# Kernel optimization log

Measured on AMD Instinct MI355X. Metric: run time of the kernel, lower is better.

The kernel has to match this reference:

```python
import jax, jax.numpy as jnp
import numpy as np

NUM_QUERIES = 300


def setup_inputs() -> dict:
    key = jax.random.key(0)
    ks = jax.random.split(key, 16)
    B, C, NC = 16, 256, 80
    s = 0.02
    return {
        "s3": jax.random.normal(ks[0], (B, C, 128, 128), jnp.float32),
        "s4": jax.random.normal(ks[1], (B, C, 64, 64), jnp.float32),
        "s5": jax.random.normal(ks[2], (B, C, 32, 32), jnp.float32),
        "w_score": jax.random.normal(ks[3], (C, NC), jnp.float32) * s,
        "b_score": jnp.zeros((NC,), jnp.float32),
        "w1": jax.random.normal(ks[4], (C, C), jnp.float32) * s,
        "b1": jnp.zeros((C,), jnp.float32),
        "w2": jax.random.normal(ks[5], (C, C), jnp.float32) * s,
        "b2": jnp.zeros((C,), jnp.float32),
        "w3": jax.random.normal(ks[6], (C, 4), jnp.float32) * s,
        "b3": jnp.zeros((4,), jnp.float32),
        "w_proj": jax.random.normal(ks[7], (C, C), jnp.float32) * s,
        "b_proj": jnp.zeros((C,), jnp.float32),
    }


def _flatten(feats):
    # each feat [B,C,H,W] -> [B,H*W,C]; concat over levels
    mems = [f.reshape(f.shape[0], f.shape[1], -1).transpose(0, 2, 1) for f in feats]
    return jnp.concatenate(mems, axis=1)


def reference(s3, s4, s5, w_score, b_score, w1, b1, w2, b2, w3, b3, w_proj, b_proj):
    memory = _flatten([s3, s4, s5])  # [B, N, C]

    # encoder heads
    enc_logits = memory @ w_score + b_score                      # [B, N, num_classes]
    h = jax.nn.relu(memory @ w1 + b1)
    h = jax.nn.relu(h @ w2 + b2)
    enc_boxes = h @ w3 + b3                                      # [B, N, 4]

    # top-k query selection: sigmoid -> per-token max class score -> topk -> gather
    scores = jax.nn.sigmoid(enc_logits).max(axis=-1)             # [B, N]
    topk_scores, topk_idx = jax.lax.top_k(scores, NUM_QUERIES)   # [B, K]
    topk_mem = jnp.take_along_axis(memory, topk_idx[:, :, None], axis=1)    # [B, K, C]
    topk_boxes = jnp.take_along_axis(enc_boxes, topk_idx[:, :, None], axis=1)  # [B, K, 4]

    tgt = topk_mem @ w_proj + b_proj                             # [B, K, C]
    ref_points = jax.nn.sigmoid(topk_boxes)                      # [B, K, 4]

    return (tgt, ref_points, enc_logits, jax.nn.sigmoid(enc_boxes), topk_idx, topk_scores)
```

## Files before the change

### kernel.cpp

```cpp
#include <hip/hip_runtime.h>
#include <math.h>

#define BATCH 16
#define CDIM 256
#define NCLS 80
#define N3 16384
#define N4 4096
#define N5 1024
#define NTOK 21504
#define KQ 300
#define KSEL 512
#define CANDMAX 1024

typedef __attribute__((ext_vector_type(8))) short short8;
typedef __attribute__((ext_vector_type(4))) float floatx4;
typedef __attribute__((ext_vector_type(16))) float floatx16;
typedef unsigned short ushort_t;

__device__ __forceinline__ float sigmoidf_(float x) {
    return 1.0f / (1.0f + __expf(-x));
}

__device__ __forceinline__ ushort_t f2bf(float f) {
    unsigned int x = __float_as_uint(f);
    unsigned int r = (x + 0x7FFFu + ((x >> 16) & 1u)) >> 16;
    return (ushort_t)r;
}

__device__ __forceinline__ float bf2f(ushort_t u) {
    return __uint_as_float((unsigned int)u << 16);
}

__device__ __forceinline__ void locate_level(
    int n, int bb,
    const float* __restrict__ s3, const float* __restrict__ s4, const float* __restrict__ s5,
    const float*& src, int& nloc, int& lsz)
{
    if (n < N3)           { src = s3 + (size_t)bb * CDIM * N3; nloc = n;           lsz = N3; }
    else if (n < N3 + N4) { src = s4 + (size_t)bb * CDIM * N4; nloc = n - N3;      lsz = N4; }
    else                  { src = s5 + (size_t)bb * CDIM * N5; nloc = n - N3 - N4; lsz = N5; }
}

__global__ __launch_bounds__(256) void prep_weights(
    const float* __restrict__ w1, const float* __restrict__ w2,
    const float* __restrict__ w_score,
    ushort_t* __restrict__ wPk)
{
    const int c = blockIdx.x;
    for (int i = threadIdx.x; i < 8192; i += 256) {
        const int f = i >> 9;
        const int e = i & 511;
        const int ln = e >> 3;
        const int j = e & 7;
        const int col = ln & 31;
        const int k = 16 * f + (ln >> 5) * 8 + j;
        float v;
        if (c < 3) {
            const int cc = 32 * c + col;
            v = (cc < NCLS) ? w_score[k * NCLS + cc] : 0.f;
        } else if (c < 11) {
            v = w1[k * 256 + (32 * (c - 3) + col)];
        } else {
            v = w2[k * 256 + (32 * (c - 11) + col)];
        }
        wPk[(size_t)c * 8192 + i] = f2bf(v);
    }
}

__global__ __launch_bounds__(256) void enc_mfma_kernel(
    const float* __restrict__ s3, const float* __restrict__ s4, const float* __restrict__ s5,
    const ushort_t* __restrict__ wPk,
    const float* __restrict__ b_score, const float* __restrict__ b1,
    const float* __restrict__ b2,
    const float* __restrict__ w3, const float* __restrict__ b3,
    float* __restrict__ out_logits, float* __restrict__ out_sboxes,
    float* __restrict__ ws_scores)
{
    __shared__ __align__(16) ushort_t ldsA[256 * 68];
    __shared__ __align__(16) float w3_s[256 * 4];
    __shared__ float smax_s[2][64];

    const int t = threadIdx.x;
    const int lane = t & 63;
    const int w = t >> 6;
    const int tw = w & 1;
    const int cw = w >> 1;
    const int ln = lane & 31;
    const int half = lane >> 5;

    const int bb = blockIdx.x / 336;
    const int tile = blockIdx.x % 336;
    const int T0 = tile * 64;

    const float* src; int nloc, lsz;
    locate_level(T0, bb, s3, s4, s5, src, nloc, lsz);

    {
        const int tokq = t & 15;
        const int kr = t >> 4;
        #pragma unroll
        for (int p = 0; p < 16; ++p) {
            const int k = p * 16 + kr;
            const float4 v = *(const float4*)(src + (size_t)k * lsz + nloc + 4 * tokq);
            const unsigned int lo = (unsigned int)f2bf(v.x) | ((unsigned int)f2bf(v.y) << 16);
            const unsigned int hi = (unsigned int)f2bf(v.z) | ((unsigned int)f2bf(v.w) << 16);
            *(uint2*)&ldsA[k * 68 + 4 * tokq] = make_uint2(lo, hi);
        }
        *(float4*)&w3_s[t * 4] = *(const float4*)(w3 + t * 4);
    }
    __syncthreads();

    short8 af[16];
    #pragma unroll
    for (int f = 0; f < 16; ++f) {
        short8 a;
        #pragma unroll
        for (int j = 0; j < 8; ++j)
            a[j] = (short)ldsA[(16 * f + 8 * half + j) * 68 + 32 * tw + ln];
        af[f] = a;
    }
    __syncthreads();

    const int gtok0 = bb * NTOK + T0 + 32 * tw;

    float smaxr[16];
    #pragma unroll
    for (int r = 0; r < 16; ++r) smaxr[r] = -1e30f;

    for (int c = cw; c < 11; c += 2) {
        const ushort_t* bp = wPk + (size_t)c * 8192;
        floatx16 acc = {0.f,0.f,0.f,0.f,0.f,0.f,0.f,0.f,0.f,0.f,0.f,0.f,0.f,0.f,0.f,0.f};
        #pragma unroll
        for (int fh = 0; fh < 2; ++fh) {
            short8 bf[8];
            #pragma unroll
            for (int f2 = 0; f2 < 8; ++f2)
                bf[f2] = *(const short8*)&bp[(8 * fh + f2) * 512 + lane * 8];
            #pragma unroll
            for (int f2 = 0; f2 < 8; ++f2)
                acc = __builtin_amdgcn_mfma_f32_32x32x16_bf16(af[8 * fh + f2], bf[f2], acc, 0, 0, 0);
        }
        if (c < 3) {
            const int col = 32 * c + ln;
            const bool valid = col < NCLS;
            const float bias = valid ? b_score[col] : 0.f;
            #pragma unroll
            for (int r = 0; r < 16; ++r) {
                const int row = (r & 3) + 8 * (r >> 2) + 4 * half;
                const float v = acc[r] + bias;
                if (valid) {
                    out_logits[(size_t)(gtok0 + row) * NCLS + col] = v;
                    smaxr[r] = fmaxf(smaxr[r], v);
                }
            }
        } else {
            const int col = 32 * (c - 3) + ln;
            const float bias = b1[col];
            #pragma unroll
            for (int r = 0; r < 16; ++r) {
                const int row = (r & 3) + 8 * (r >> 2) + 4 * half;
                const int tok = 32 * tw + row;
                const float v = fmaxf(acc[r] + bias, 0.f);
                ldsA[tok * 256 + ((((col >> 3) ^ (row & 7)) << 3) | (col & 7))] = f2bf(v);
            }
        }
    }

    #pragma unroll
    for (int r = 0; r < 16; ++r) {
        float m = smaxr[r];
        m = fmaxf(m, __shfl_xor(m, 1));
        m = fmaxf(m, __shfl_xor(m, 2));
        m = fmaxf(m, __shfl_xor(m, 4));
        m = fmaxf(m, __shfl_xor(m, 8));
        m = fmaxf(m, __shfl_xor(m, 16));
        if (ln == 0) {
            const int row = (r & 3) + 8 * (r >> 2) + 4 * half;
            smax_s[cw][32 * tw + row] = m;
        }
    }
    __syncthreads();

    if (t < 64) {
        const float m = fmaxf(smax_s[0][t], smax_s[1][t]);
        ws_scores[bb * NTOK + T0 + t] = sigmoidf_(m);
    }

    {
        const int tok = 32 * tw + ln;
        #pragma unroll
        for (int f = 0; f < 16; ++f) {
            const int chnk = 2 * f + half;
            af[f] = *(const short8*)&ldsA[tok * 256 + ((chnk ^ (tok & 7)) << 3)];
        }
    }
    __syncthreads();

    for (int c = 11 + cw; c < 19; c += 2) {
        const ushort_t* bp = wPk + (size_t)c * 8192;
        floatx16 acc = {0.f,0.f,0.f,0.f,0.f,0.f,0.f,0.f,0.f,0.f,0.f,0.f,0.f,0.f,0.f,0.f};
        #pragma unroll
        for (int fh = 0; fh < 2; ++fh) {
            short8 bf[8];
            #pragma unroll
            for (int f2 = 0; f2 < 8; ++f2)
                bf[f2] = *(const short8*)&bp[(8 * fh + f2) * 512 + lane * 8];
            #pragma unroll
            for (int f2 = 0; f2 < 8; ++f2)
                acc = __builtin_amdgcn_mfma_f32_32x32x16_bf16(af[8 * fh + f2], bf[f2], acc, 0, 0, 0);
        }
        const int col = 32 * (c - 11) + ln;
        const float bias = b2[col];
        #pragma unroll
        for (int r = 0; r < 16; ++r) {
            const int row = (r & 3) + 8 * (r >> 2) + 4 * half;
            const int tok = 32 * tw + row;
            const float v = fmaxf(acc[r] + bias, 0.f);
            ldsA[tok * 256 + ((((col >> 3) ^ (row & 7)) << 3) | (col & 7))] = f2bf(v);
        }
    }
    __syncthreads();

    {
        const int tok = t >> 2;
        const int j = t & 3;
        float acc = b3[j];
        #pragma unroll
        for (int ch = 0; ch < 32; ++ch) {
            const short8 v = *(const short8*)&ldsA[tok * 256 + ((ch ^ (tok & 7)) << 3)];
            #pragma unroll
            for (int jj = 0; jj < 8; ++jj)
                acc = fmaf(bf2f((ushort_t)v[jj]), w3_s[(ch * 8 + jj) * 4 + j], acc);
        }
        out_sboxes[(size_t)(bb * NTOK + T0 + tok) * 4 + j] = sigmoidf_(acc);
    }
}

__global__ __launch_bounds__(256) void select_kernel(
    const float* __restrict__ scores,
    int* __restrict__ cand_idx, unsigned int* __restrict__ cand_cnt)
{
    const int bb = blockIdx.x;
    const int t = threadIdx.x;
    const int lane = t & 63;
    const float* s = scores + bb * NTOK;

    __shared__ unsigned int hist[256];
    __shared__ unsigned int prefix_s, rem_s, cnt_s;

    unsigned int prefix = 0, mask = 0;
    int remaining = KSEL;
    for (int pass = 0; pass < 4; pass++) {
        const int shift = 24 - 8 * pass;
        hist[t] = 0;
        __syncthreads();
        for (int n = t; n < NTOK; n += 256) {
            const unsigned int key = __float_as_uint(s[n]);
            const bool pred = ((key & mask) == prefix);
            const unsigned int bin = pred ? ((key >> shift) & 255u) : 0xFFFFu;
            const unsigned long long alive = __ballot(pred);
            if (alive) {
                const int leader = __builtin_ctzll(alive);
                const unsigned int lbin = (unsigned int)__shfl((int)bin, leader);
                const unsigned long long match = __ballot(pred && bin == lbin);
                if (lane == leader)
                    atomicAdd(&hist[lbin], (unsigned int)__popcll(match));
                else if (pred && bin != lbin)
                    atomicAdd(&hist[bin], 1u);
            }
        }
        __syncthreads();
        if (t == 0) {
            int rem = remaining; unsigned int bsel = 0;
            for (int bin = 255; bin >= 0; bin--) {
                int c = (int)hist[bin];
                if (c >= rem) { bsel = (unsigned int)bin; break; }
                rem -= c;
            }
            prefix_s = prefix | (bsel << shift);
            rem_s = (unsigned int)rem;
        }
        __syncthreads();
        prefix = prefix_s; remaining = (int)rem_s;
        mask |= 0xFFu << shift;
        __syncthreads();
    }
    const unsigned int Tkey = prefix;

    if (t == 0) cnt_s = 0;
    __syncthreads();
    for (int n = t; n < NTOK; n += 256) {
        const unsigned int key = __float_as_uint(s[n]);
        const bool pred = (key >= Tkey);
        const unsigned long long m = __ballot(pred);
        if (m) {
            const int leader = __builtin_ctzll(m);
            unsigned int base = 0;
            if (lane == leader) base = atomicAdd(&cnt_s, (unsigned int)__popcll(m));
            base = (unsigned int)__shfl((int)base, leader);
            if (pred) {
                const unsigned int pos =
                    base + (unsigned int)__popcll(m & ((1ull << lane) - 1ull));
                if (pos < CANDMAX) cand_idx[bb * CANDMAX + pos] = n;
            }
        }
    }
    __syncthreads();
    if (t == 0) {
        unsigned int c = cnt_s; if (c > CANDMAX) c = CANDMAX;
        cand_cnt[bb] = c;
    }
}

__global__ __launch_bounds__(256) void rescore_kernel(
    const float* __restrict__ s3, const float* __restrict__ s4, const float* __restrict__ s5,
    const float* __restrict__ w_score, const float* __restrict__ b_score,
    const int* __restrict__ cand_idx, const unsigned int* __restrict__ cand_cnt,
    double* __restrict__ cand_score)
{
    __shared__ float mrow[4][CDIM];
    const int t = threadIdx.x;
    const int w = t >> 6;
    const int lane = t & 63;
    const int bb = blockIdx.x / (CANDMAX / 4);
    const int c  = (blockIdx.x % (CANDMAX / 4)) * 4 + w;
    const unsigned int cnt = cand_cnt[bb];
    const bool active = (unsigned int)c < cnt;

    int n = 0;
    if (active) n = cand_idx[bb * CANDMAX + c];
    if (active) {
        const float* src; int nloc, lsz;
        locate_level(n, bb, s3, s4, s5, src, nloc, lsz);
        #pragma unroll
        for (int j = 0; j < 4; j++)
            mrow[w][4 * lane + j] = src[(size_t)(4 * lane + j) * lsz + nloc];
    }
    __syncthreads();

    if (active) {
        double acc0 = (double)b_score[lane];
        double acc1 = (lane < 16) ? (double)b_score[64 + lane] : -1.0e300;
        for (int k = 0; k < CDIM; k++) {
            const double m = (double)mrow[w][k];
            acc0 += m * (double)w_score[k * NCLS + lane];
            if (lane < 16) acc1 += m * (double)w_score[k * NCLS + 64 + lane];
        }
        double mx = fmax(acc0, acc1);
        mx = fmax(mx, __shfl_xor(mx, 1));
        mx = fmax(mx, __shfl_xor(mx, 2));
        mx = fmax(mx, __shfl_xor(mx, 4));
        mx = fmax(mx, __shfl_xor(mx, 8));
        mx = fmax(mx, __shfl_xor(mx, 16));
        mx = fmax(mx, __shfl_xor(mx, 32));
        if (lane == 0) cand_score[bb * CANDMAX + c] = mx;
    }
}

__global__ __launch_bounds__(256) void fsort_kernel(
    const double* __restrict__ cand_score, const int* __restrict__ cand_idx,
    const unsigned int* __restrict__ cand_cnt,
    float* __restrict__ out_idx_f, float* __restrict__ out_scores,
    int* __restrict__ ws_idx)
{
    __shared__ double ss[CANDMAX];
    __shared__ int    ii[CANDMAX];
    const int bb = blockIdx.x;
    const int t = threadIdx.x;
    const unsigned int cnt = cand_cnt[bb];

    for (int i = t; i < CANDMAX; i += 256) {
        if ((unsigned int)i < cnt) {
            ss[i] = cand_score[bb * CANDMAX + i];
            ii[i] = cand_idx[bb * CANDMAX + i];
        } else {
            ss[i] = -1.0e300;
            ii[i] = 0x7FFFFFFF;
        }
    }
    __syncthreads();

    for (int ksz = 2; ksz <= CANDMAX; ksz <<= 1) {
        for (int j = ksz >> 1; j > 0; j >>= 1) {
            #pragma unroll
            for (int p = 0; p < CANDMAX / 256; p++) {
                const int i = p * 256 + t;
                const int ixj = i ^ j;
                if (ixj > i) {
                    double sa = ss[i], sb = ss[ixj];
                    int ia = ii[i], ib = ii[ixj];
                    const bool up = ((i & ksz) != 0);
                    const bool agtb = (sa > sb) || (sa == sb && ia < ib);
                    if (agtb == up) { ss[i] = sb; ss[ixj] = sa; ii[i] = ib; ii[ixj] = ia; }
                }
            }
            __syncthreads();
        }
    }

    for (int q = t; q < KQ; q += 256) {
        const double x = ss[q];
        const int idx = ii[q];
        out_scores[bb * KQ + q] = (float)(1.0 / (1.0 + exp(-x)));
        out_idx_f[bb * KQ + q] = (float)idx;
        ws_idx[bb * KQ + q] = idx;
    }
}

__global__ __launch_bounds__(256) void gather_proj_kernel(
    const float* __restrict__ s3, const float* __restrict__ s4, const float* __restrict__ s5,
    const float* __restrict__ w_proj, const float* __restrict__ b_proj,
    const int* __restrict__ ws_idx, const float* __restrict__ out_sboxes,
    float* __restrict__ out_tgt, float* __restrict__ out_ref)
{
    __shared__ float memQ[20][CDIM];
    __shared__ int qidx[20];
    const int t = threadIdx.x;
    const int bb = blockIdx.x / 15;
    const int tile = blockIdx.x % 15;
    const int q0 = tile * 20;

    if (t < 20) qidx[t] = ws_idx[bb * KQ + q0 + t];
    __syncthreads();

    #pragma unroll 4
    for (int q = 0; q < 20; q++) {
        const int n = qidx[q];
        const float* src; int nloc, lsz;
        locate_level(n, bb, s3, s4, s5, src, nloc, lsz);
        memQ[q][t] = src[(size_t)t * lsz + nloc];
    }
    __syncthreads();

    const int j = t;
    float acc[20];
    #pragma unroll
    for (int q = 0; q < 20; q++) acc[q] = b_proj[j];
    for (int k = 0; k < CDIM; k++) {
        const float w = w_proj[(size_t)k * CDIM + j];
        #pragma unroll
        for (int q = 0; q < 20; q++) acc[q] = fmaf(memQ[q][k], w, acc[q]);
    }
    #pragma unroll
    for (int q = 0; q < 20; q++)
        out_tgt[(size_t)(bb * KQ + q0 + q) * CDIM + j] = acc[q];

    if (t < 80) {
        const int q = t >> 2, c = t & 3;
        const int n = qidx[q];
        out_ref[(size_t)(bb * KQ + q0 + q) * 4 + c] =
            out_sboxes[(size_t)(bb * NTOK + n) * 4 + c];
    }
}

extern "C" void kernel_launch(void* const* d_in, const int* in_sizes, int n_in,
                              void* d_out, int out_size, void* d_ws, size_t ws_size,
                              hipStream_t stream) {
    const float* s3      = (const float*)d_in[0];
    const float* s4      = (const float*)d_in[1];
    const float* s5      = (const float*)d_in[2];
    const float* w_score = (const float*)d_in[3];
    const float* b_score = (const float*)d_in[4];
    const float* w1      = (const float*)d_in[5];
    const float* b1      = (const float*)d_in[6];
    const float* w2      = (const float*)d_in[7];
    const float* b2      = (const float*)d_in[8];
    const float* w3      = (const float*)d_in[9];
    const float* b3      = (const float*)d_in[10];
    const float* w_proj  = (const float*)d_in[11];
    const float* b_proj  = (const float*)d_in[12];

    float* out = (float*)d_out;
    float* out_tgt    = out;
    float* out_ref    = out + 1228800;
    float* out_logits = out + 1248000;
    float* out_sboxes = out + 28773120;
    float* out_idx    = out + 30149376;
    float* out_scores = out + 30154176;

    char* ws = (char*)d_ws;
    float*        ws_scores  = (float*)(ws + 0);
    double*       cand_score = (double*)(ws + 1376256);
    int*          cand_idx   = (int*)(ws + 1507328);
    unsigned int* cand_cnt   = (unsigned int*)(ws + 1572864);
    int*          ws_idx     = (int*)(ws + 1573120);
    ushort_t*     wPk        = (ushort_t*)(ws + 1592576);

    prep_weights<<<19, 256, 0, stream>>>(w1, w2, w_score, wPk);

    enc_mfma_kernel<<<BATCH * 336, 256, 0, stream>>>(
        s3, s4, s5, wPk, b_score, b1, b2, w3, b3,
        out_logits, out_sboxes, ws_scores);

    select_kernel<<<BATCH, 256, 0, stream>>>(ws_scores, cand_idx, cand_cnt);

    rescore_kernel<<<BATCH * (CANDMAX / 4), 256, 0, stream>>>(
        s3, s4, s5, w_score, b_score, cand_idx, cand_cnt, cand_score);

    fsort_kernel<<<BATCH, 256, 0, stream>>>(
        cand_score, cand_idx, cand_cnt, out_idx, out_scores, ws_idx);

    gather_proj_kernel<<<BATCH * 15, 256, 0, stream>>>(
        s3, s4, s5, w_proj, b_proj, ws_idx, out_sboxes, out_tgt, out_ref);
}
```

Measured before the change: 1.038 ms.

## Double encoder token tile, reuse weight fragments across two MFMA tiles, MFMA box head

The encoder kernel now handles 128 tokens per block instead of 64. Each wave loads its activation fragments straight from global memory into registers, skipping the LDS transpose, and applies every loaded weight fragment to two 32-token MFMA tiles, which halves weight traffic per token. The final 256→4 box projection now runs as a single zero-padded MFMA, using a packed bf16 w3 copy built in prep_weights, in place of the scalar FMA loop. The costs are much higher register pressure (launch bounds set to 2 blocks per CU), half as many blocks, and strided scalar global loads for the activations.

New measurement: 1.315 ms. 26.8% more time.

```diff
diff --git a/kernel.cpp b/kernel.cpp
--- a/kernel.cpp
+++ b/kernel.cpp
@@ -11,11 +11,15 @@
 #define KQ 300
 #define KSEL 512
 #define CANDMAX 1024
+#define TBLK 128
+#define NBLK 168
 
 typedef __attribute__((ext_vector_type(8))) short short8;
-typedef __attribute__((ext_vector_type(4))) float floatx4;
 typedef __attribute__((ext_vector_type(16))) float floatx16;
 typedef unsigned short ushort_t;
+
+#define ZEROV {0.f,0.f,0.f,0.f,0.f,0.f,0.f,0.f,0.f,0.f,0.f,0.f,0.f,0.f,0.f,0.f}
+#define H1S(tok, col) (((tok) << 8) + (((((col) >> 3) ^ ((tok) & 7)) << 3) | ((col) & 7)))
 
 __device__ __forceinline__ float sigmoidf_(float x) {
     return 1.0f / (1.0f + __expf(-x));
@@ -27,10 +31,6 @@
     return (ushort_t)r;
 }
 
-__device__ __forceinline__ float bf2f(ushort_t u) {
-    return __uint_as_float((unsigned int)u << 16);
-}
-
 __device__ __forceinline__ void locate_level(
     int n, int bb,
     const float* __restrict__ s3, const float* __restrict__ s4, const float* __restrict__ s5,
@@ -43,42 +43,43 @@
 
 __global__ __launch_bounds__(256) void prep_weights(
     const float* __restrict__ w1, const float* __restrict__ w2,
-    const float* __restrict__ w_score,
-    ushort_t* __restrict__ wPk)
+    const float* __restrict__ w_score, const float* __restrict__ w3,
+    ushort_t* __restrict__ wPk, ushort_t* __restrict__ w3Pk)
 {
     const int c = blockIdx.x;
     for (int i = threadIdx.x; i < 8192; i += 256) {
         const int f = i >> 9;
         const int e = i & 511;
-        const int ln = e >> 3;
+        const int lni = e >> 3;
         const int j = e & 7;
-        const int col = ln & 31;
-        const int k = 16 * f + (ln >> 5) * 8 + j;
+        const int col = lni & 31;
+        const int k = 16 * f + (lni >> 5) * 8 + j;
         float v;
         if (c < 3) {
             const int cc = 32 * c + col;
             v = (cc < NCLS) ? w_score[k * NCLS + cc] : 0.f;
         } else if (c < 11) {
             v = w1[k * 256 + (32 * (c - 3) + col)];
+        } else if (c < 19) {
+            v = w2[k * 256 + (32 * (c - 11) + col)];
         } else {
-            v = w2[k * 256 + (32 * (c - 11) + col)];
-        }
-        wPk[(size_t)c * 8192 + i] = f2bf(v);
-    }
-}
-
-__global__ __launch_bounds__(256) void enc_mfma_kernel(
+            v = (col < 4) ? w3[k * 4 + col] : 0.f;
+        }
+        ushort_t* dst = (c < 19) ? (wPk + (size_t)c * 8192) : w3Pk;
+        dst[i] = f2bf(v);
+    }
+}
+
+__global__ __launch_bounds__(256, 2) void enc_mfma_kernel(
     const float* __restrict__ s3, const float* __restrict__ s4, const float* __restrict__ s5,
-    const ushort_t* __restrict__ wPk,
+    const ushort_t* __restrict__ wPk, const ushort_t* __restrict__ w3Pk,
     const float* __restrict__ b_score, const float* __restrict__ b1,
-    const float* __restrict__ b2,
-    const float* __restrict__ w3, const float* __restrict__ b3,
+    const float* __restrict__ b2, const float* __restrict__ b3,
     float* __restrict__ out_logits, float* __restrict__ out_sboxes,
     float* __restrict__ ws_scores)
 {
-    __shared__ __align__(16) ushort_t ldsA[256 * 68];
-    __shared__ __align__(16) float w3_s[256 * 4];
-    __shared__ float smax_s[2][64];
+    __shared__ __align__(16) ushort_t h1b[TBLK * 256];
+    __shared__ float smax_s[2][TBLK];
 
     const int t = threadIdx.x;
     const int lane = t & 63;
@@ -88,151 +89,167 @@
     const int ln = lane & 31;
     const int half = lane >> 5;
 
-    const int bb = blockIdx.x / 336;
-    const int tile = blockIdx.x % 336;
-    const int T0 = tile * 64;
+    const int bb = blockIdx.x / NBLK;
+    const int tile = blockIdx.x % NBLK;
+    const int T0 = tile * TBLK;
 
     const float* src; int nloc, lsz;
     locate_level(T0, bb, s3, s4, s5, src, nloc, lsz);
 
-    {
-        const int tokq = t & 15;
-        const int kr = t >> 4;
-        #pragma unroll
-        for (int p = 0; p < 16; ++p) {
-            const int k = p * 16 + kr;
-            const float4 v = *(const float4*)(src + (size_t)k * lsz + nloc + 4 * tokq);
-            const unsigned int lo = (unsigned int)f2bf(v.x) | ((unsigned int)f2bf(v.y) << 16);
-            const unsigned int hi = (unsigned int)f2bf(v.z) | ((unsigned int)f2bf(v.w) << 16);
-            *(uint2*)&ldsA[k * 68 + 4 * tokq] = make_uint2(lo, hi);
-        }
-        *(float4*)&w3_s[t * 4] = *(const float4*)(w3 + t * 4);
-    }
-    __syncthreads();
-
-    short8 af[16];
-    #pragma unroll
-    for (int f = 0; f < 16; ++f) {
-        short8 a;
-        #pragma unroll
-        for (int j = 0; j < 8; ++j)
-            a[j] = (short)ldsA[(16 * f + 8 * half + j) * 68 + 32 * tw + ln];
-        af[f] = a;
-    }
-    __syncthreads();
-
-    const int gtok0 = bb * NTOK + T0 + 32 * tw;
-
-    float smaxr[16];
-    #pragma unroll
-    for (int r = 0; r < 16; ++r) smaxr[r] = -1e30f;
-
-    for (int c = cw; c < 11; c += 2) {
-        const ushort_t* bp = wPk + (size_t)c * 8192;
-        floatx16 acc = {0.f,0.f,0.f,0.f,0.f,0.f,0.f,0.f,0.f,0.f,0.f,0.f,0.f,0.f,0.f,0.f};
-        #pragma unroll
-        for (int fh = 0; fh < 2; ++fh) {
-            short8 bf[8];
-            #pragma unroll
-            for (int f2 = 0; f2 < 8; ++f2)
-                bf[f2] = *(const short8*)&bp[(8 * fh + f2) * 512 + lane * 8];
-            #pragma unroll
-            for (int f2 = 0; f2 < 8; ++f2)
-                acc = __builtin_amdgcn_mfma_f32_32x32x16_bf16(af[8 * fh + f2], bf[f2], acc, 0, 0, 0);
-        }
-        if (c < 3) {
-            const int col = 32 * c + ln;
-            const bool valid = col < NCLS;
-            const float bias = valid ? b_score[col] : 0.f;
+    short8 af[2][16];
+    #pragma unroll
+    for (int tt = 0; tt < 2; ++tt) {
+        const float* colp = src + (size_t)(nloc + 64 * tw + 32 * tt + ln);
+        #pragma unroll
+        for (int f = 0; f < 16; ++f) {
+            const size_t kb = (size_t)(16 * f + 8 * half);
+            float r[8];
+            #pragma unroll
+            for (int j = 0; j < 8; ++j) r[j] = colp[(kb + j) * (size_t)lsz];
+            short8 a;
+            #pragma unroll
+            for (int j = 0; j < 8; ++j) a[j] = (short)f2bf(r[j]);
+            af[tt][f] = a;
+        }
+    }
+
+    const int gt00 = bb * NTOK + T0;
+
+    auto mm2 = [&](const ushort_t* bp, floatx16& a0, floatx16& a1) {
+        short8 blo[8], bhi[8];
+        #pragma unroll
+        for (int f2 = 0; f2 < 8; ++f2)
+            blo[f2] = *(const short8*)&bp[(size_t)f2 * 512 + lane * 8];
+        #pragma unroll
+        for (int f2 = 0; f2 < 8; ++f2)
+            bhi[f2] = *(const short8*)&bp[(size_t)(8 + f2) * 512 + lane * 8];
+        #pragma unroll
+        for (int f2 = 0; f2 < 8; ++f2) {
+            a0 = __builtin_amdgcn_mfma_f32_32x32x16_bf16(af[0][f2], blo[f2], a0, 0, 0, 0);
+            a1 = __builtin_amdgcn_mfma_f32_32x32x16_bf16(af[1][f2], blo[f2], a1, 0, 0, 0);
+        }
+        #pragma unroll
+        for (int f2 = 0; f2 < 8; ++f2) {
+            a0 = __builtin_amdgcn_mfma_f32_32x32x16_bf16(af[0][8 + f2], bhi[f2], a0, 0, 0, 0);
+            a1 = __builtin_amdgcn_mfma_f32_32x32x16_bf16(af[1][8 + f2], bhi[f2], a1, 0, 0, 0);
+        }
+    };
+
+    #pragma unroll
+    for (int q = 0; q < 2; ++q) {
+        const int c = cw + 2 * q;
+        if (c > 2) continue;
+        floatx16 a0 = ZEROV, a1 = ZEROV;
+        mm2(wPk + (size_t)c * 8192, a0, a1);
+        const int col = 32 * c + ln;
+        const bool valid = col < NCLS;
+        const float bias = b_score[valid ? col : 0];
+        #pragma unroll
+        for (int tt = 0; tt < 2; ++tt) {
+            const floatx16 acc = tt ? a1 : a0;
             #pragma unroll
             for (int r = 0; r < 16; ++r) {
                 const int row = (r & 3) + 8 * (r >> 2) + 4 * half;
-                const float v = acc[r] + bias;
-                if (valid) {
-                    out_logits[(size_t)(gtok0 + row) * NCLS + col] = v;
-                    smaxr[r] = fmaxf(smaxr[r], v);
+                float v = valid ? (acc[r] + bias) : -1e30f;
+                if (valid)
+                    out_logits[(size_t)(gt00 + 64 * tw + 32 * tt + row) * NCLS + col] = v;
+                v = fmaxf(v, __shfl_xor(v, 1));
+                v = fmaxf(v, __shfl_xor(v, 2));
+                v = fmaxf(v, __shfl_xor(v, 4));
+                v = fmaxf(v, __shfl_xor(v, 8));
+                v = fmaxf(v, __shfl_xor(v, 16));
+                if (ln == 0) {
+                    float* slot = &smax_s[cw][64 * tw + 32 * tt + row];
+                    *slot = (q == 0) ? v : fmaxf(*slot, v);
                 }
             }
-        } else {
-            const int col = 32 * (c - 3) + ln;
-            const float bias = b1[col];
+        }
+    }
+
+    #pragma unroll
+    for (int q = 0; q < 4; ++q) {
+        const int c = 3 + cw + 2 * q;
+        floatx16 a0 = ZEROV, a1 = ZEROV;
+        mm2(wPk + (size_t)c * 8192, a0, a1);
+        const int col = 32 * (c - 3) + ln;
+        const float bias = b1[col];
+        #pragma unroll
+        for (int tt = 0; tt < 2; ++tt) {
+            const floatx16 acc = tt ? a1 : a0;
             #pragma unroll
             for (int r = 0; r < 16; ++r) {
                 const int row = (r & 3) + 8 * (r >> 2) + 4 * half;
-                const int tok = 32 * tw + row;
-                const float v = fmaxf(acc[r] + bias, 0.f);
-                ldsA[tok * 256 + ((((col >> 3) ^ (row & 7)) << 3) | (col & 7))] = f2bf(v);
-            }
-        }
-    }
-
-    #pragma unroll
-    for (int r = 0; r < 16; ++r) {
-        float m = smaxr[r];
-        m = fmaxf(m, __shfl_xor(m, 1));
-        m = fmaxf(m, __shfl_xor(m, 2));
-        m = fmaxf(m, __shfl_xor(m, 4));
-        m = fmaxf(m, __shfl_xor(m, 8));
-        m = fmaxf(m, __shfl_xor(m, 16));
-        if (ln == 0) {
-            const int row = (r & 3) + 8 * (r >> 2) + 4 * half;
-            smax_s[cw][32 * tw + row] = m;
-        }
-    }
-    __syncthreads();
-
-    if (t < 64) {
-        const float m = fmaxf(smax_s[0][t], smax_s[1][t]);
-        ws_scores[bb * NTOK + T0 + t] = sigmoidf_(m);
-    }
-
-    {
-        const int tok = 32 * tw + ln;
+                const int tok = 64 * tw + 32 * tt + row;
+                h1b[H1S(tok, col)] = f2bf(fmaxf(acc[r] + bias, 0.f));
+            }
+        }
+    }
+    __syncthreads();
+
+    if (t < TBLK)
+        ws_scores[gt00 + t] = sigmoidf_(fmaxf(smax_s[0][t], smax_s[1][t]));
+
+    #pragma unroll
+    for (int tt = 0; tt < 2; ++tt) {
+        const int tok = 64 * tw + 32 * tt + ln;
         #pragma unroll
         for (int f = 0; f < 16; ++f) {
-            const int chnk = 2 * f + half;
-            af[f] = *(const short8*)&ldsA[tok * 256 + ((chnk ^ (tok & 7)) << 3)];
-        }
-    }
-    __syncthreads();
-
-    for (int c = 11 + cw; c < 19; c += 2) {
-        const ushort_t* bp = wPk + (size_t)c * 8192;
-        floatx16 acc = {0.f,0.f,0.f,0.f,0.f,0.f,0.f,0.f,0.f,0.f,0.f,0.f,0.f,0.f,0.f,0.f};
-        #pragma unroll
-        for (int fh = 0; fh < 2; ++fh) {
-            short8 bf[8];
-            #pragma unroll
-            for (int f2 = 0; f2 < 8; ++f2)
-                bf[f2] = *(const short8*)&bp[(8 * fh + f2) * 512 + lane * 8];
-            #pragma unroll
-            for (int f2 = 0; f2 < 8; ++f2)
-                acc = __builtin_amdgcn_mfma_f32_32x32x16_bf16(af[8 * fh + f2], bf[f2], acc, 0, 0, 0);
-        }
+            const int ch = 2 * f + half;
+            af[tt][f] = *(const short8*)&h1b[(tok << 8) + ((ch ^ (tok & 7)) << 3)];
+        }
+    }
+    __syncthreads();
+
+    #pragma unroll
+    for (int q = 0; q < 4; ++q) {
+        const int c = 11 + cw + 2 * q;
+        floatx16 a0 = ZEROV, a1 = ZEROV;
+        mm2(wPk + (size_t)c * 8192, a0, a1);
         const int col = 32 * (c - 11) + ln;
         const float bias = b2[col];
         #pragma unroll
-        for (int r = 0; r < 16; ++r) {
-            const int row = (r & 3) + 8 * (r >> 2) + 4 * half;
-            const int tok = 32 * tw + row;
-            const float v = fmaxf(acc[r] + bias, 0.f);
-            ldsA[tok * 256 + ((((col >> 3) ^ (row & 7)) << 3) | (col & 7))] = f2bf(v);
+        for (int tt = 0; tt < 2; ++tt) {
+            const floatx16 acc = tt ? a1 : a0;
+            #pragma unroll
+            for (int r = 0; r < 16; ++r) {
+                const int row = (r & 3) + 8 * (r >> 2) + 4 * half;
+                const int tok = 64 * tw + 32 * tt + row;
+                h1b[H1S(tok, col)] = f2bf(fmaxf(acc[r] + bias, 0.f));
+            }
         }
     }
     __syncthreads();
 
     {
-        const int tok = t >> 2;
-        const int j = t & 3;
-        float acc = b3[j];
-        #pragma unroll
-        for (int ch = 0; ch < 32; ++ch) {
-            const short8 v = *(const short8*)&ldsA[tok * 256 + ((ch ^ (tok & 7)) << 3)];
-            #pragma unroll
-            for (int jj = 0; jj < 8; ++jj)
-                acc = fmaf(bf2f((ushort_t)v[jj]), w3_s[(ch * 8 + jj) * 4 + j], acc);
-        }
-        out_sboxes[(size_t)(bb * NTOK + T0 + tok) * 4 + j] = sigmoidf_(acc);
+        const int tokb = 64 * tw + 32 * cw;
+        const int tok = tokb + ln;
+        #pragma unroll
+        for (int f = 0; f < 16; ++f) {
+            const int ch = 2 * f + half;
+            af[0][f] = *(const short8*)&h1b[(tok << 8) + ((ch ^ (tok & 7)) << 3)];
+        }
+        short8 blo[8], bhi[8];
+        #pragma unroll
+        for (int f2 = 0; f2 < 8; ++f2)
+            blo[f2] = *(const short8*)&w3Pk[(size_t)f2 * 512 + lane * 8];
+        #pragma unroll
+        for (int f2 = 0; f2 < 8; ++f2)
+            bhi[f2] = *(const short8*)&w3Pk[(size_t)(8 + f2) * 512 + lane * 8];
+        floatx16 acc = ZEROV;
+        #pragma unroll
+        for (int f2 = 0; f2 < 8; ++f2)
+            acc = __builtin_amdgcn_mfma_f32_32x32x16_bf16(af[0][f2], blo[f2], acc, 0, 0, 0);
+        #pragma unroll
+        for (int f2 = 0; f2 < 8; ++f2)
+            acc = __builtin_amdgcn_mfma_f32_32x32x16_bf16(af[0][8 + f2], bhi[f2], acc, 0, 0, 0);
+        const float b3v = b3[ln & 3];
+        if (ln < 4) {
+            #pragma unroll
+            for (int r = 0; r < 16; ++r) {
+                const int row = (r & 3) + 8 * (r >> 2) + 4 * half;
+                out_sboxes[(size_t)(gt00 + tokb + row) * 4 + ln] = sigmoidf_(acc[r] + b3v);
+            }
+        }
     }
 }
 
@@ -485,11 +502,12 @@
     unsigned int* cand_cnt   = (unsigned int*)(ws + 1572864);
     int*          ws_idx     = (int*)(ws + 1573120);
     ushort_t*     wPk        = (ushort_t*)(ws + 1592576);
-
-    prep_weights<<<19, 256, 0, stream>>>(w1, w2, w_score, wPk);
-
-    enc_mfma_kernel<<<BATCH * 336, 256, 0, stream>>>(
-        s3, s4, s5, wPk, b_score, b1, b2, w3, b3,
+    ushort_t*     w3Pk       = (ushort_t*)(ws + 1376256);
+
+    prep_weights<<<20, 256, 0, stream>>>(w1, w2, w_score, w3, wPk, w3Pk);
+
+    enc_mfma_kernel<<<BATCH * NBLK, 256, 0, stream>>>(
+        s3, s4, s5, wPk, w3Pk, b_score, b1, b2, b3,
         out_logits, out_sboxes, ws_scores);
 
     select_kernel<<<BATCH, 256, 0, stream>>>(ws_scores, cand_idx, cand_cnt);
```
